# Kernel optimization log

Hardware: AMD Instinct MI355X
Metric: run time of the kernel (lower is better)

The kernel has to match this reference:

```python
import jax, jax.numpy as jnp
import numpy as np

N = 50000   # nodes
E = 600000  # edges per relation
H = 4       # heads
DH = 32     # head dim (out_feat // num_heads)
D = 128     # in_feat == out_feat
NEG_SLOPE = 0.2


def setup_inputs() -> dict:
    key = jax.random.key(0)
    ks = jax.random.split(key, 13)
    x = jax.random.normal(ks[0], (N, D), jnp.float32)
    src_r0 = jax.random.randint(ks[1], (E,), 0, N, jnp.int32)
    dst_r0 = jax.random.randint(ks[2], (E,), 0, N, jnp.int32)
    src_r1 = jax.random.randint(ks[3], (E,), 0, N, jnp.int32)
    dst_r1 = jax.random.randint(ks[4], (E,), 0, N, jnp.int32)
    s = 0.05  # keep activations moderate (xavier-like scale)
    W_r0 = jax.random.normal(ks[5], (D, H * DH), jnp.float32) * s
    attn_l_r0 = jax.random.normal(ks[6], (H, DH), jnp.float32) * s
    attn_r_r0 = jax.random.normal(ks[7], (H, DH), jnp.float32) * s
    W_r1 = jax.random.normal(ks[8], (D, H * DH), jnp.float32) * s
    attn_l_r1 = jax.random.normal(ks[9], (H, DH), jnp.float32) * s
    attn_r_r1 = jax.random.normal(ks[10], (H, DH), jnp.float32) * s
    loop_weight = jax.random.normal(ks[11], (D, D), jnp.float32) * s
    h_bias = jnp.zeros((D,), jnp.float32)
    return {"x": x, "src_r0": src_r0, "dst_r0": dst_r0, "src_r1": src_r1,
            "dst_r1": dst_r1, "W_r0": W_r0, "attn_l_r0": attn_l_r0,
            "attn_r_r0": attn_r_r0, "W_r1": W_r1, "attn_l_r1": attn_l_r1,
            "attn_r_r1": attn_r_r1, "loop_weight": loop_weight, "h_bias": h_bias}


def _gat_rel(x, src, dst, W, attn_l, attn_r):
    """DGL GATConv for one relation: fc -> per-node attn scalars -> edge
    leaky_relu -> per-dst softmax -> weighted scatter-sum. Heads flattened."""
    feat = (x @ W).reshape(-1, H, DH)                 # [N, H, DH]
    el = jnp.einsum('nhd,hd->nh', feat, attn_l)       # [N, H]
    er = jnp.einsum('nhd,hd->nh', feat, attn_r)       # [N, H]
    e = jax.nn.leaky_relu(el[src] + er[dst], NEG_SLOPE)  # [E, H]
    # edge softmax per destination node, per head (numerically stable)
    m = jax.ops.segment_max(e, dst, num_segments=N)   # [N, H]
    ex = jnp.exp(e - m[dst])                          # [E, H]
    z = jax.ops.segment_sum(ex, dst, num_segments=N)  # [N, H]
    a = ex / z[dst]                                   # [E, H]
    msg = a[:, :, None] * feat[src]                   # [E, H, DH]
    out = jax.ops.segment_sum(msg, dst, num_segments=N)  # [N, H, DH]
    return out.reshape(-1, H * DH)                    # [N, D] (concat heads)


def reference(x, src_r0, dst_r0, src_r1, dst_r1, W_r0, attn_l_r0, attn_r_r0,
              W_r1, attn_l_r1, attn_r_r1, loop_weight, h_bias):
    # HeteroGraphConv with default 'sum' aggregation across relations
    h = _gat_rel(x, src_r0, dst_r0, W_r0, attn_l_r0, attn_r_r0)
    h = h + _gat_rel(x, src_r1, dst_r1, W_r1, attn_l_r1, attn_r_r1)
    # self-loop linear + bias + activation (dropout p=0.0 is identity)
    h = h + x @ loop_weight + h_bias
    return jax.nn.relu(h)
```

## Files before the change

### kernel.cpp

```cpp
#include <hip/hip_runtime.h>
#include <math.h>


#define CAP 48
#define NB 256
#define BCAP 2752
#define BIN_EDGES 4096

typedef __attribute__((ext_vector_type(8))) short short8v;
typedef __attribute__((ext_vector_type(4))) float float4v;

__device__ __forceinline__ unsigned short f2bf(float f) {
  unsigned int u = __float_as_uint(f);
  unsigned int r = (u + 0x7fffu + ((u >> 16) & 1u)) >> 16;
  return (unsigned short)r;
}
__device__ __forceinline__ float2 bfpair(unsigned int u) {
  float2 r;
  r.x = __uint_as_float(u << 16);
  r.y = __uint_as_float(u & 0xffff0000u);
  return r;
}

__global__ __launch_bounds__(256) void prep_kernel(
    const float* __restrict__ W0, const float* __restrict__ W1,
    const float* __restrict__ WL,
    const float* __restrict__ al0, const float* __restrict__ ar0,
    const float* __restrict__ al1, const float* __restrict__ ar1,
    unsigned short* __restrict__ Wtall, int* __restrict__ gcnt)
{
  const int t = threadIdx.x;
  if (blockIdx.x == 0) {
    gcnt[t] = 0;
    gcnt[t + 256] = 0;
  }
  const int j = blockIdx.x * 256 + t;
  if (j < 4096) {
    const int rel = j >> 11;
    const int q = j & 2047;
    const int n = q >> 4;
    const int k0 = (q & 15) * 8;
    const float* W = rel ? W1 : W0;
    unsigned short o[8];
#pragma unroll
    for (int u = 0; u < 8; ++u) o[u] = f2bf(W[(size_t)(k0 + u) * 128 + n]);
    *(short8v*)&Wtall[(size_t)rel * 18432 + n * 128 + k0] = *(short8v*)o;
  } else if (j < 4352) {
    const int e = j - 4096;
    const int rel = e >> 7;
    const int q = e & 127;
    const int cIdx = q >> 4;
    const int isr = cIdx >> 2;
    const int h = cIdx & 3;
    const int k0 = (q & 15) * 8;
    const float* W = rel ? W1 : W0;
    const float* av = isr ? (rel ? ar1 : ar0) : (rel ? al1 : al0);
    unsigned short o[8];
#pragma unroll
    for (int u = 0; u < 8; ++u) {
      float s = 0.f;
#pragma unroll
      for (int d = 0; d < 32; ++d)
        s += W[(size_t)(k0 + u) * 128 + h * 32 + d] * av[h * 32 + d];
      o[u] = f2bf(s);
    }
    *(short8v*)&Wtall[(size_t)rel * 18432 + (128 + cIdx) * 128 + k0] = *(short8v*)o;
  } else if (j < 4608) {
    const int e = j - 4352;
    const int rel = e >> 7;
    const int q = e & 127;
    const int cIdx = 136 + (q >> 4);
    const int k0 = (q & 15) * 8;
    const short8v z = {0,0,0,0,0,0,0,0};
    *(short8v*)&Wtall[(size_t)rel * 18432 + cIdx * 128 + k0] = z;
  } else if (j < 6656) {
    const int e = j - 4608;
    const int n = e >> 4;
    const int k0 = (e & 15) * 8;
    unsigned short o[8];
#pragma unroll
    for (int u = 0; u < 8; ++u) o[u] = f2bf(WL[(size_t)(k0 + u) * 128 + n]);
    *(short8v*)&Wtall[(size_t)2 * 18432 + n * 128 + k0] = *(short8v*)o;
  }
}

__global__ __launch_bounds__(256) void bin_kernel(
    const int* __restrict__ src0, const int* __restrict__ dst0,
    const int* __restrict__ src1, const int* __restrict__ dst1,
    unsigned int* __restrict__ bpair, int* __restrict__ gcnt,
    int E, int width, int nbin)
{
  __shared__ int smem[512];
  int* cnt = smem;
  int* gb  = smem + NB;
  const int t = threadIdx.x;
  const int bid = blockIdx.x;
  const int rel = (bid >= nbin) ? 1 : 0;
  const int ib  = rel ? (bid - nbin) : bid;
  const int* srcA = rel ? src1 : src0;
  const int* dstA = rel ? dst1 : dst0;
  const int base = ib * BIN_EDGES;
  const int cntE = min(E - base, BIN_EDGES);

  cnt[t] = 0;
  __syncthreads();

  unsigned int epack[16]; int eb[16], epos[16];
#pragma unroll
  for (int q = 0; q < 16; ++q) {
    const int ei = q * 256 + t;
    if (ei < cntE) {
      const int s = srcA[base + ei];
      const int d = dstA[base + ei];
      const int b = d / width;
      const int ld = d - b * width;
      epack[q] = (unsigned int)s | ((unsigned int)ld << 16);
      eb[q] = b;
      epos[q] = atomicAdd(&cnt[b], 1);
    } else {
      eb[q] = -1;
    }
  }
  __syncthreads();
  gb[t] = atomicAdd(&gcnt[rel * NB + t], cnt[t]);
  __syncthreads();
#pragma unroll
  for (int q = 0; q < 16; ++q) {
    if (eb[q] >= 0) {
      const int slot = gb[eb[q]] + epos[q];
      if (slot < BCAP)
        bpair[(size_t)(rel * NB + eb[q]) * BCAP + slot] = epack[q];
    }
  }
}

__global__ __launch_bounds__(256) void gemm_ell_kernel(
    const float* __restrict__ x, const unsigned short* __restrict__ Wtall,
    unsigned short* __restrict__ f0, unsigned short* __restrict__ f1,
    unsigned short* __restrict__ xl,
    float* __restrict__ el0, float* __restrict__ er0,
    float* __restrict__ el1, float* __restrict__ er1,
    const unsigned int* __restrict__ bpair, const int* __restrict__ gcnt,
    int* __restrict__ deg, unsigned short* __restrict__ ell0,
    unsigned short* __restrict__ ell1,
    int N, int width, int ngemm)
{
  __shared__ int ldeg[256];

  if ((int)blockIdx.x < ngemm) {
    const int wave = threadIdx.x >> 6, lane = threadIdx.x & 63;
    const int lr = lane & 15, lk = lane >> 4;
    const int row0 = blockIdx.x * 128 + wave * 32;

    short8v a[2][4];
#pragma unroll
    for (int mf = 0; mf < 2; ++mf) {
      const int r = row0 + mf * 16 + lr;
#pragma unroll
      for (int kc = 0; kc < 4; ++kc) {
        if (r < N) {
          const float* xp = &x[(size_t)r * 128 + kc * 32 + lk * 8];
          float4 u = *(const float4*)xp;
          float4 v = *(const float4*)(xp + 4);
          unsigned short o[8];
          o[0]=f2bf(u.x); o[1]=f2bf(u.y); o[2]=f2bf(u.z); o[3]=f2bf(u.w);
          o[4]=f2bf(v.x); o[5]=f2bf(v.y); o[6]=f2bf(v.z); o[7]=f2bf(v.w);
          a[mf][kc] = *(short8v*)o;
        } else {
          a[mf][kc] = (short8v){0,0,0,0,0,0,0,0};
        }
      }
    }

#pragma unroll
    for (int w = 0; w < 3; ++w) {
      const unsigned short* Wp = Wtall + (size_t)w * 18432;
      const int NF = (w < 2) ? 9 : 8;
      float4v acc[2][9];
#pragma unroll
      for (int mf = 0; mf < 2; ++mf)
#pragma unroll
        for (int nf = 0; nf < 9; ++nf) acc[mf][nf] = (float4v){0.f, 0.f, 0.f, 0.f};
      for (int nf = 0; nf < NF; ++nf) {
        const unsigned short* Bp = &Wp[(size_t)(nf * 16 + lr) * 128];
#pragma unroll
        for (int kc = 0; kc < 4; ++kc) {
          const short8v b = *(const short8v*)&Bp[kc * 32 + lk * 8];
          acc[0][nf] = __builtin_amdgcn_mfma_f32_16x16x32_bf16(a[0][kc], b, acc[0][nf], 0, 0, 0);
          acc[1][nf] = __builtin_amdgcn_mfma_f32_16x16x32_bf16(a[1][kc], b, acc[1][nf], 0, 0, 0);
        }
      }

      unsigned short* dstp = (w == 0) ? f0 : (w == 1) ? f1 : xl;
#pragma unroll
      for (int mf = 0; mf < 2; ++mf) {
#pragma unroll
        for (int nf = 0; nf < 8; ++nf) {
          const int col = nf * 16 + lr;
#pragma unroll
          for (int j = 0; j < 4; ++j) {
            const int row = row0 + mf * 16 + lk * 4 + j;
            if (row < N) dstp[(size_t)row * 128 + col] = f2bf(acc[mf][nf][j]);
          }
        }
      }
      if (w < 2 && lr < 8) {
        float* ep = (lr < 4) ? (w ? el1 : el0) : (w ? er1 : er0);
        const int h = lr & 3;
#pragma unroll
        for (int mf = 0; mf < 2; ++mf)
#pragma unroll
          for (int j = 0; j < 4; ++j) {
            const int row = row0 + mf * 16 + lk * 4 + j;
            if (row < N) ep[row * 4 + h] = acc[mf][8][j];
          }
      }
    }
  } else {
    const int bid = blockIdx.x - ngemm;
    const int rel = bid >> 8;
    const int b = bid & 255;
    const int t = threadIdx.x;
    const int d0 = b * width;
    if (t < width) ldeg[t] = 0;
    __syncthreads();
    const int count = min(gcnt[rel * NB + b], BCAP);
    unsigned short* ell = rel ? ell1 : ell0;
    const unsigned int* bp = &bpair[(size_t)(rel * NB + b) * BCAP];
    for (int i = t; i < count; i += 256) {
      const unsigned int v = bp[i];
      const int src = (int)(v & 0xFFFFu);
      const int ld = (int)(v >> 16);
      const int slot = atomicAdd(&ldeg[ld], 1);
      if (slot < CAP) ell[(size_t)(d0 + ld) * CAP + slot] = (unsigned short)src;
    }
    __syncthreads();
    if (t < width && d0 + t < N) deg[rel * N + d0 + t] = ldeg[t];
  }
}

__global__ __launch_bounds__(256) void gat_aggregate_kernel(
    const unsigned short* __restrict__ f0, const unsigned short* __restrict__ f1,
    const unsigned short* __restrict__ xl,
    const float* __restrict__ el0, const float* __restrict__ er0,
    const float* __restrict__ el1, const float* __restrict__ er1,
    const int* __restrict__ deg,
    const unsigned short* __restrict__ ell0, const unsigned short* __restrict__ ell1,
    const float* __restrict__ bias, float* __restrict__ out, int N)
{
  __shared__ float p_lds[4][2][4][16];
  const int wid  = threadIdx.x >> 6;
  const int lane = threadIdx.x & 63;
  const int n = blockIdx.x * 4 + wid;
  if (n >= N) return;
  const int h  = lane >> 4;
  const int il = lane & 15;
  const int c  = lane * 2;

  const int rs0 = (int)ell0[(size_t)n * CAP + il];
  const int rs1 = (int)ell1[(size_t)n * CAP + il];
  const int d0 = min(deg[n], CAP);
  const int d1 = min(deg[N + n], CAP);
  const float er0h = er0[n * 4 + h];
  const float er1h = er1[n * 4 + h];

  const bool v0 = il < d0, v1 = il < d1;
  const int s0 = v0 ? rs0 : 0;
  const int s1 = v1 ? rs1 : 0;

  const float elv0 = el0[s0 * 4 + h];
  const float elv1 = el1[s1 * 4 + h];

  unsigned int fu0[16], fu1[16];
#pragma unroll
  for (int i = 0; i < 16; ++i) {
    const int s = __builtin_amdgcn_readlane(s0, i);
    fu0[i] = *(const unsigned int*)&f0[(size_t)s * 128 + c];
  }
#pragma unroll
  for (int i = 0; i < 16; ++i) {
    const int s = __builtin_amdgcn_readlane(s1, i);
    fu1[i] = *(const unsigned int*)&f1[(size_t)s * 128 + c];
  }

  float m0, sum0, m1, sum1;
  {
    float e = elv0 + er0h;  e = e > 0.f ? e : 0.2f * e;
    float ev = v0 ? e : -INFINITY;
    float cm = ev;
    cm = fmaxf(cm, __shfl_xor(cm, 1)); cm = fmaxf(cm, __shfl_xor(cm, 2));
    cm = fmaxf(cm, __shfl_xor(cm, 4)); cm = fmaxf(cm, __shfl_xor(cm, 8));
    const float p = __expf(ev - cm);
    float cs = p;
    cs += __shfl_xor(cs, 1); cs += __shfl_xor(cs, 2);
    cs += __shfl_xor(cs, 4); cs += __shfl_xor(cs, 8);
    m0 = cm; sum0 = cs;
    p_lds[wid][0][h][il] = p;
  }
  {
    float e = elv1 + er1h;  e = e > 0.f ? e : 0.2f * e;
    float ev = v1 ? e : -INFINITY;
    float cm = ev;
    cm = fmaxf(cm, __shfl_xor(cm, 1)); cm = fmaxf(cm, __shfl_xor(cm, 2));
    cm = fmaxf(cm, __shfl_xor(cm, 4)); cm = fmaxf(cm, __shfl_xor(cm, 8));
    const float p = __expf(ev - cm);
    float cs = p;
    cs += __shfl_xor(cs, 1); cs += __shfl_xor(cs, 2);
    cs += __shfl_xor(cs, 4); cs += __shfl_xor(cs, 8);
    m1 = cm; sum1 = cs;
    p_lds[wid][1][h][il] = p;
  }

  float ax0 = 0.f, ay0 = 0.f;
  {
    float p16[16];
    *(float4*)&p16[0]  = *(const float4*)&p_lds[wid][0][h][0];
    *(float4*)&p16[4]  = *(const float4*)&p_lds[wid][0][h][4];
    *(float4*)&p16[8]  = *(const float4*)&p_lds[wid][0][h][8];
    *(float4*)&p16[12] = *(const float4*)&p_lds[wid][0][h][12];
    float axa=0.f, aya=0.f, axb=0.f, ayb=0.f;
#pragma unroll
    for (int i = 0; i < 16; i += 2) {
      const float2 fa = bfpair(fu0[i]);
      const float2 fb2 = bfpair(fu0[i+1]);
      axa += p16[i]*fa.x;   aya += p16[i]*fa.y;
      axb += p16[i+1]*fb2.x; ayb += p16[i+1]*fb2.y;
    }
    ax0 = axa + axb; ay0 = aya + ayb;
  }
  float ax1 = 0.f, ay1 = 0.f;
  {
    float p16[16];
    *(float4*)&p16[0]  = *(const float4*)&p_lds[wid][1][h][0];
    *(float4*)&p16[4]  = *(const float4*)&p_lds[wid][1][h][4];
    *(float4*)&p16[8]  = *(const float4*)&p_lds[wid][1][h][8];
    *(float4*)&p16[12] = *(const float4*)&p_lds[wid][1][h][12];
    float axa=0.f, aya=0.f, axb=0.f, ayb=0.f;
#pragma unroll
    for (int i = 0; i < 16; i += 2) {
      const float2 fa = bfpair(fu1[i]);
      const float2 fb2 = bfpair(fu1[i+1]);
      axa += p16[i]*fa.x;   aya += p16[i]*fa.y;
      axb += p16[i+1]*fb2.x; ayb += p16[i+1]*fb2.y;
    }
    ax1 = axa + axb; ay1 = aya + ayb;
  }

  auto tail = [&](const unsigned short* ellp, const float* elp, float erh,
                  int d, const unsigned short* fbp, float& m, float& sum,
                  float& ax, float& ay, int slot) {
    for (int base = 16; base < d; base += 16) {
      const bool valid = (base + il) < d;
      int sv = (int)ellp[(size_t)n * CAP + base + il];
      sv = valid ? sv : 0;
      const float elv = elp[sv * 4 + h];
      unsigned int fu[16];
#pragma unroll
      for (int i = 0; i < 16; ++i) {
        const int s = __builtin_amdgcn_readlane(sv, i);
        fu[i] = *(const unsigned int*)&fbp[(size_t)s * 128 + c];
      }
      float e = elv + erh; e = e > 0.f ? e : 0.2f * e;
      const float ev = valid ? e : -INFINITY;
      float cm = ev;
      cm = fmaxf(cm, __shfl_xor(cm, 1)); cm = fmaxf(cm, __shfl_xor(cm, 2));
      cm = fmaxf(cm, __shfl_xor(cm, 4)); cm = fmaxf(cm, __shfl_xor(cm, 8));
      const float mn = fmaxf(m, cm);
      const float scale = __expf(m - mn);
      const float p = __expf(ev - mn);
      float cs = p;
      cs += __shfl_xor(cs, 1); cs += __shfl_xor(cs, 2);
      cs += __shfl_xor(cs, 4); cs += __shfl_xor(cs, 8);
      sum = sum * scale + cs;
      m = mn;
      p_lds[wid][slot][h][il] = p;
      float p16[16];
      *(float4*)&p16[0]  = *(const float4*)&p_lds[wid][slot][h][0];
      *(float4*)&p16[4]  = *(const float4*)&p_lds[wid][slot][h][4];
      *(float4*)&p16[8]  = *(const float4*)&p_lds[wid][slot][h][8];
      *(float4*)&p16[12] = *(const float4*)&p_lds[wid][slot][h][12];
      float axa=0.f, aya=0.f;
#pragma unroll
      for (int i = 0; i < 16; ++i) {
        const float2 f = bfpair(fu[i]);
        axa += p16[i]*f.x; aya += p16[i]*f.y;
      }
      ax = ax * scale + axa;
      ay = ay * scale + aya;
    }
  };
  if (d0 > 16) tail(ell0, el0, er0h, d0, f0, m0, sum0, ax0, ay0, 0);
  if (d1 > 16) tail(ell1, el1, er1h, d1, f1, m1, sum1, ax1, ay1, 1);

  float ox = 0.f, oy = 0.f;
  if (d0 > 0) { const float inv = 1.f / sum0; ox += ax0 * inv; oy += ay0 * inv; }
  if (d1 > 0) { const float inv = 1.f / sum1; ox += ax1 * inv; oy += ay1 * inv; }
  const float2 xlv = bfpair(*(const unsigned int*)&xl[(size_t)n * 128 + c]);
  const float2 bv  = *(const float2*)&bias[c];
  ox += xlv.x + bv.x;
  oy += xlv.y + bv.y;
  float2 res;
  res.x = fmaxf(ox, 0.f);
  res.y = fmaxf(oy, 0.f);
  *(float2*)&out[(size_t)n * 128 + c] = res;
}

extern "C" void kernel_launch(void* const* d_in, const int* in_sizes, int n_in,
                              void* d_out, int out_size, void* d_ws, size_t ws_size,
                              hipStream_t stream)
{
  const int N = in_sizes[0] / 128;
  const int E = in_sizes[1];

  const float* x    = (const float*)d_in[0];
  const int* src0   = (const int*)d_in[1];
  const int* dst0   = (const int*)d_in[2];
  const int* src1   = (const int*)d_in[3];
  const int* dst1   = (const int*)d_in[4];
  const float* W0   = (const float*)d_in[5];
  const float* al0  = (const float*)d_in[6];
  const float* ar0  = (const float*)d_in[7];
  const float* W1   = (const float*)d_in[8];
  const float* al1  = (const float*)d_in[9];
  const float* ar1  = (const float*)d_in[10];
  const float* WL   = (const float*)d_in[11];
  const float* bias = (const float*)d_in[12];
  float* out = (float*)d_out;

  char* p = (char*)d_ws;
  auto alloc = [&](size_t bytes) { char* r = p; p += (bytes + 255) & ~(size_t)255; return r; };
  unsigned short* f0 = (unsigned short*)alloc((size_t)N * 128 * 2);
  unsigned short* f1 = (unsigned short*)alloc((size_t)N * 128 * 2);
  unsigned short* xl = (unsigned short*)alloc((size_t)N * 128 * 2);
  float* el0 = (float*)alloc((size_t)N * 4 * 4);
  float* er0 = (float*)alloc((size_t)N * 4 * 4);
  float* el1 = (float*)alloc((size_t)N * 4 * 4);
  float* er1 = (float*)alloc((size_t)N * 4 * 4);
  int* deg   = (int*)alloc((size_t)2 * N * 4);
  unsigned short* ell0 = (unsigned short*)alloc((size_t)CAP * N * 2);
  unsigned short* ell1 = (unsigned short*)alloc((size_t)CAP * N * 2);
  unsigned int* bpair = (unsigned int*)alloc((size_t)2 * NB * BCAP * 4);
  int* gcnt  = (int*)alloc((size_t)2 * NB * 4);
  unsigned short* Wtall = (unsigned short*)alloc((size_t)(2 * 144 + 128) * 128 * 2);

  const int width = (N + NB - 1) / NB;
  const int ngemm = (N + 127) / 128;
  const int nbin  = (E + BIN_EDGES - 1) / BIN_EDGES;

  prep_kernel<<<26, 256, 0, stream>>>(
      W0, W1, WL, al0, ar0, al1, ar1, Wtall, gcnt);

  bin_kernel<<<2 * nbin, 256, 0, stream>>>(
      src0, dst0, src1, dst1, bpair, gcnt, E, width, nbin);

  gemm_ell_kernel<<<ngemm + 2 * NB, 256, 0, stream>>>(
      x, Wtall, f0, f1, xl, el0, er0, el1, er1,
      bpair, gcnt, deg, ell0, ell1, N, width, ngemm);

  gat_aggregate_kernel<<<(N + 3) / 4, 256, 0, stream>>>(
      f0, f1, xl, el0, er0, el1, er1, deg, ell0, ell1, bias, out, N);
}
```

Measured before the change: 138.8 us.

## Fuse GEMM with edge binning and stage weights in swizzled LDS

Edge binning now runs inside the GEMM kernel as extra blocks, and ELL construction moves to its own kernel, so binning overlaps the dense projection instead of preceding it. Each GEMM block also stages each weight matrix into a 36KB LDS buffer with an XOR swizzle and reads B fragments from LDS rather than global memory. The cost is larger LDS use, which may lower occupancy, extra block-level barriers per weight matrix, and removal of full unrolling on the outer w loop.

```diff
diff --git a/kernel.cpp b/kernel.cpp
--- a/kernel.cpp
+++ b/kernel.cpp
@@ -84,68 +84,18 @@
   }
 }
 
-__global__ __launch_bounds__(256) void bin_kernel(
+__global__ __launch_bounds__(256) void gemm_bin_kernel(
+    const float* __restrict__ x, const unsigned short* __restrict__ Wtall,
     const int* __restrict__ src0, const int* __restrict__ dst0,
     const int* __restrict__ src1, const int* __restrict__ dst1,
-    unsigned int* __restrict__ bpair, int* __restrict__ gcnt,
-    int E, int width, int nbin)
-{
-  __shared__ int smem[512];
-  int* cnt = smem;
-  int* gb  = smem + NB;
-  const int t = threadIdx.x;
-  const int bid = blockIdx.x;
-  const int rel = (bid >= nbin) ? 1 : 0;
-  const int ib  = rel ? (bid - nbin) : bid;
-  const int* srcA = rel ? src1 : src0;
-  const int* dstA = rel ? dst1 : dst0;
-  const int base = ib * BIN_EDGES;
-  const int cntE = min(E - base, BIN_EDGES);
-
-  cnt[t] = 0;
-  __syncthreads();
-
-  unsigned int epack[16]; int eb[16], epos[16];
-#pragma unroll
-  for (int q = 0; q < 16; ++q) {
-    const int ei = q * 256 + t;
-    if (ei < cntE) {
-      const int s = srcA[base + ei];
-      const int d = dstA[base + ei];
-      const int b = d / width;
-      const int ld = d - b * width;
-      epack[q] = (unsigned int)s | ((unsigned int)ld << 16);
-      eb[q] = b;
-      epos[q] = atomicAdd(&cnt[b], 1);
-    } else {
-      eb[q] = -1;
-    }
-  }
-  __syncthreads();
-  gb[t] = atomicAdd(&gcnt[rel * NB + t], cnt[t]);
-  __syncthreads();
-#pragma unroll
-  for (int q = 0; q < 16; ++q) {
-    if (eb[q] >= 0) {
-      const int slot = gb[eb[q]] + epos[q];
-      if (slot < BCAP)
-        bpair[(size_t)(rel * NB + eb[q]) * BCAP + slot] = epack[q];
-    }
-  }
-}
-
-__global__ __launch_bounds__(256) void gemm_ell_kernel(
-    const float* __restrict__ x, const unsigned short* __restrict__ Wtall,
     unsigned short* __restrict__ f0, unsigned short* __restrict__ f1,
     unsigned short* __restrict__ xl,
     float* __restrict__ el0, float* __restrict__ er0,
     float* __restrict__ el1, float* __restrict__ er1,
-    const unsigned int* __restrict__ bpair, const int* __restrict__ gcnt,
-    int* __restrict__ deg, unsigned short* __restrict__ ell0,
-    unsigned short* __restrict__ ell1,
-    int N, int width, int ngemm)
+    unsigned int* __restrict__ bpair, int* __restrict__ gcnt,
+    int N, int E, int width, int ngemm, int nbin)
 {
-  __shared__ int ldeg[256];
+  __shared__ char smem_raw[36864];
 
   if ((int)blockIdx.x < ngemm) {
     const int wave = threadIdx.x >> 6, lane = threadIdx.x & 63;
@@ -172,20 +122,35 @@
       }
     }
 
-#pragma unroll
     for (int w = 0; w < 3; ++w) {
-      const unsigned short* Wp = Wtall + (size_t)w * 18432;
+      __syncthreads();
+      {
+        const unsigned short* Wp = Wtall + (size_t)w * 18432;
+        const int nElem = (w < 2) ? 18432 : 16384;
+        for (int i = threadIdx.x * 8; i < nElem; i += 2048) {
+          const short8v v = *(const short8v*)&Wp[i];
+          const int row = i >> 7;
+          const int byte = (i * 2) ^ ((row & 7) << 4);
+          *(short8v*)&smem_raw[byte] = v;
+        }
+      }
+      __syncthreads();
+
       const int NF = (w < 2) ? 9 : 8;
       float4v acc[2][9];
 #pragma unroll
       for (int mf = 0; mf < 2; ++mf)
 #pragma unroll
         for (int nf = 0; nf < 9; ++nf) acc[mf][nf] = (float4v){0.f, 0.f, 0.f, 0.f};
+#pragma unroll 3
       for (int nf = 0; nf < NF; ++nf) {
-        const unsigned short* Bp = &Wp[(size_t)(nf * 16 + lr) * 128];
+        const int row = nf * 16 + lr;
+        const int rb = row * 256;
+        const int sw = (row & 7) << 4;
 #pragma unroll
         for (int kc = 0; kc < 4; ++kc) {
-          const short8v b = *(const short8v*)&Bp[kc * 32 + lk * 8];
+          const int byte = (rb + kc * 64 + lk * 16) ^ sw;
+          const short8v b = *(const short8v*)&smem_raw[byte];
           acc[0][nf] = __builtin_amdgcn_mfma_f32_16x16x32_bf16(a[0][kc], b, acc[0][nf], 0, 0, 0);
           acc[1][nf] = __builtin_amdgcn_mfma_f32_16x16x32_bf16(a[1][kc], b, acc[1][nf], 0, 0, 0);
         }
@@ -217,26 +182,74 @@
       }
     }
   } else {
+    int* cnt = (int*)smem_raw;
+    int* gb  = ((int*)smem_raw) + NB;
+    const int t = threadIdx.x;
     const int bid = blockIdx.x - ngemm;
-    const int rel = bid >> 8;
-    const int b = bid & 255;
-    const int t = threadIdx.x;
-    const int d0 = b * width;
-    if (t < width) ldeg[t] = 0;
+    const int rel = (bid >= nbin) ? 1 : 0;
+    const int ib  = rel ? (bid - nbin) : bid;
+    const int* srcA = rel ? src1 : src0;
+    const int* dstA = rel ? dst1 : dst0;
+    const int base = ib * BIN_EDGES;
+    const int cntE = min(E - base, BIN_EDGES);
+
+    cnt[t] = 0;
     __syncthreads();
-    const int count = min(gcnt[rel * NB + b], BCAP);
-    unsigned short* ell = rel ? ell1 : ell0;
-    const unsigned int* bp = &bpair[(size_t)(rel * NB + b) * BCAP];
-    for (int i = t; i < count; i += 256) {
-      const unsigned int v = bp[i];
-      const int src = (int)(v & 0xFFFFu);
-      const int ld = (int)(v >> 16);
-      const int slot = atomicAdd(&ldeg[ld], 1);
-      if (slot < CAP) ell[(size_t)(d0 + ld) * CAP + slot] = (unsigned short)src;
+
+    unsigned int epack[16]; int eb[16], epos[16];
+#pragma unroll
+    for (int q = 0; q < 16; ++q) {
+      const int ei = q * 256 + t;
+      if (ei < cntE) {
+        const int s = srcA[base + ei];
+        const int d = dstA[base + ei];
+        const int b = d / width;
+        const int ld = d - b * width;
+        epack[q] = (unsigned int)s | ((unsigned int)ld << 16);
+        eb[q] = b;
+        epos[q] = atomicAdd(&cnt[b], 1);
+      } else {
+        eb[q] = -1;
+      }
     }
     __syncthreads();
-    if (t < width && d0 + t < N) deg[rel * N + d0 + t] = ldeg[t];
-  }
+    gb[t] = atomicAdd(&gcnt[rel * NB + t], cnt[t]);
+    __syncthreads();
+#pragma unroll
+    for (int q = 0; q < 16; ++q) {
+      if (eb[q] >= 0) {
+        const int slot = gb[eb[q]] + epos[q];
+        if (slot < BCAP)
+          bpair[(size_t)(rel * NB + eb[q]) * BCAP + slot] = epack[q];
+      }
+    }
+  }
+}
+
+__global__ __launch_bounds__(256) void ell_build_kernel(
+    const unsigned int* __restrict__ bpair, const int* __restrict__ gcnt,
+    int* __restrict__ deg, unsigned short* __restrict__ ell0,
+    unsigned short* __restrict__ ell1, int N, int width)
+{
+  __shared__ int ldeg[256];
+  const int rel = blockIdx.x >> 8;
+  const int b = blockIdx.x & 255;
+  const int t = threadIdx.x;
+  const int d0 = b * width;
+  if (t < width) ldeg[t] = 0;
+  __syncthreads();
+  const int count = min(gcnt[rel * NB + b], BCAP);
+  unsigned short* ell = rel ? ell1 : ell0;
+  const unsigned int* bp = &bpair[(size_t)(rel * NB + b) * BCAP];
+  for (int i = t; i < count; i += 256) {
+    const unsigned int v = bp[i];
+    const int src = (int)(v & 0xFFFFu);
+    const int ld = (int)(v >> 16);
+    const int slot = atomicAdd(&ldeg[ld], 1);
+    if (slot < CAP) ell[(size_t)(d0 + ld) * CAP + slot] = (unsigned short)src;
+  }
+  __syncthreads();
+  if (t < width && d0 + t < N) deg[rel * N + d0 + t] = ldeg[t];
 }
 
 __global__ __launch_bounds__(256) void gat_aggregate_kernel(
@@ -450,12 +463,12 @@
   prep_kernel<<<26, 256, 0, stream>>>(
       W0, W1, WL, al0, ar0, al1, ar1, Wtall, gcnt);
 
-  bin_kernel<<<2 * nbin, 256, 0, stream>>>(
-      src0, dst0, src1, dst1, bpair, gcnt, E, width, nbin);
-
-  gemm_ell_kernel<<<ngemm + 2 * NB, 256, 0, stream>>>(
-      x, Wtall, f0, f1, xl, el0, er0, el1, er1,
-      bpair, gcnt, deg, ell0, ell1, N, width, ngemm);
+  gemm_bin_kernel<<<ngemm + 2 * nbin, 256, 0, stream>>>(
+      x, Wtall, src0, dst0, src1, dst1,
+      f0, f1, xl, el0, er0, el1, er1, bpair, gcnt, N, E, width, ngemm, nbin);
+
+  ell_build_kernel<<<2 * NB, 256, 0, stream>>>(
+      bpair, gcnt, deg, ell0, ell1, N, width);
 
   gat_aggregate_kernel<<<(N + 3) / 4, 256, 0, stream>>>(
       f0, f1, xl, el0, er0, el1, er1, deg, ell0, ell1, bias, out, N);
```

Measured after the change: 193.1 us. 39.1% more time.
